# Kernel optimization log

Measured on AMD Instinct MI355X. Metric: run time of the kernel, lower is better.

The kernel has to match this reference:

```python
import jax, jax.numpy as jnp
import numpy as np

D = 1024
N_HEADS = 16
HEAD_DIM = D // N_HEADS
EPS = 1e-09


def setup_inputs() -> dict:
    key = jax.random.key(0)
    ks = jax.random.split(key, 8)
    s = 0.02
    return {
        "x": jax.random.normal(ks[0], (2, 2048, D), jnp.float32),
        "Wq": jax.random.normal(ks[1], (D, D), jnp.float32) * s,
        "Wk": jax.random.normal(ks[2], (D, D), jnp.float32) * s,
        "Wv": jax.random.normal(ks[3], (D, D), jnp.float32) * s,
        "Wo": jax.random.normal(ks[4], (D, D), jnp.float32) * s,
        "W_up": jax.random.normal(ks[5], (4 * D, D), jnp.float32) * s,
        "W_down": jax.random.normal(ks[6], (D, 4 * D), jnp.float32) * s,
        "ln1_mean_scale": jnp.zeros((D,), jnp.float32),
        "ln1_std_scale": jnp.ones((D,), jnp.float32),
        "ln2_mean_scale": jnp.zeros((D,), jnp.float32),
        "ln2_std_scale": jnp.ones((D,), jnp.float32),
    }


def _ln(x, mean_scale, std_scale):
    mean = jnp.mean(x, axis=-1, keepdims=True)
    # torch .var() defaults to unbiased (ddof=1)
    std = jnp.sqrt(jnp.var(x, axis=-1, keepdims=True, ddof=1) + EPS)
    return (x - mean) / std * std_scale + mean_scale


def _attention(x, Wq, Wk, Wv, Wo):
    B, S, _ = x.shape
    # nn.Linear(bias=False): y = x @ W.T
    def heads(W):
        return (x @ W.T).reshape(B, S, N_HEADS, HEAD_DIM).transpose(0, 2, 1, 3)
    Q, K, V = heads(Wq), heads(Wk), heads(Wv)
    scale = jnp.sqrt(jnp.asarray(HEAD_DIM, Q.dtype))
    logits = jnp.einsum('bhqd,bhkd->bhqk', Q, K) / scale  # [B,H,S,S]
    causal = jnp.tril(jnp.ones((S, S), bool))
    logits = jnp.where(causal, logits, -jnp.inf)
    A = jax.nn.softmax(logits, axis=-1)
    preout = jnp.einsum('bhqk,bhkd->bhqd', A, V)  # [B,H,S,hd]
    # Wo.weight.T reshaped to (n_heads, d_head, d_model); per-head out then sum
    W_O = Wo.T.reshape(N_HEADS, HEAD_DIM, D)
    return jnp.einsum('bhsd,hdm->bsm', preout, W_O)


def _mlp(x, W_up, W_down):
    mid = jax.nn.gelu(x @ W_up.T, approximate=False)
    return mid @ W_down.T


def reference(x, Wq, Wk, Wv, Wo, W_up, W_down,
              ln1_mean_scale, ln1_std_scale, ln2_mean_scale, ln2_std_scale):
    x = x + _attention(_ln(x, ln1_mean_scale, ln1_std_scale), Wq, Wk, Wv, Wo)
    x = x + _mlp(_ln(x, ln2_mean_scale, ln2_std_scale), W_up, W_down)
    return x
```

## Files before the change

kernel.cpp:

```cpp
#include <hip/hip_runtime.h>
#include <hip/hip_bf16.h>
#include <cstdint>
#include <cstddef>

#define D_MODEL 1024
#define SEQ     2048
#define NTOK    4096
#define NH      16
#define HD      64

typedef __attribute__((ext_vector_type(8))) short sh8;
typedef __attribute__((ext_vector_type(4))) float f32x4;

#define GLL(g, s) __builtin_amdgcn_global_load_lds(                                   \
    (const __attribute__((address_space(1))) void*)(g),                               \
    (__attribute__((address_space(3))) void*)(s), 16, 0, 0)

__device__ __forceinline__ unsigned short f2b(float f) {
  union { float f; unsigned u; } v; v.f = f;
  unsigned r = v.u + 0x7FFFu + ((v.u >> 16) & 1u);
  return (unsigned short)(r >> 16);
}
__device__ __forceinline__ float b2f(unsigned short h) {
  union { unsigned u; float f; } v; v.u = ((unsigned)h) << 16;
  return v.f;
}

__global__ __launch_bounds__(256) void cast6_kernel(
    const float* __restrict__ q, const float* __restrict__ k, const float* __restrict__ v,
    const float* __restrict__ o, const float* __restrict__ u, const float* __restrict__ d,
    unsigned short* __restrict__ oq, unsigned short* __restrict__ ok,
    unsigned short* __restrict__ ov, unsigned short* __restrict__ oo,
    unsigned short* __restrict__ ou, unsigned short* __restrict__ od) {
  int bid = blockIdx.x;
  const float* src; unsigned short* dst; int base;
  if      (bid < 1024) { src = q; dst = oq; base = bid; }
  else if (bid < 2048) { src = k; dst = ok; base = bid - 1024; }
  else if (bid < 3072) { src = v; dst = ov; base = bid - 2048; }
  else if (bid < 4096) { src = o; dst = oo; base = bid - 3072; }
  else if (bid < 8192) { src = u; dst = ou; base = bid - 4096; }
  else                 { src = d; dst = od; base = bid - 8192; }
  int i = base * 1024 + threadIdx.x * 4;
  float4 vv = *(const float4*)(src + i);
  ushort4 w;
  w.x = f2b(vv.x); w.y = f2b(vv.y); w.z = f2b(vv.z); w.w = f2b(vv.w);
  *(ushort4*)(dst + i) = w;
}

__global__ __launch_bounds__(256) void ln_kernel(const float* __restrict__ x,
                                                 const float* __restrict__ msc,
                                                 const float* __restrict__ ssc,
                                                 unsigned short* __restrict__ out) {
  const int t = blockIdx.x;
  const int tid = threadIdx.x;
  const float4 v = ((const float4*)(x + (size_t)t * D_MODEL))[tid];
  float s = v.x + v.y + v.z + v.w;
  float q = v.x * v.x + v.y * v.y + v.z * v.z + v.w * v.w;
  #pragma unroll
  for (int off = 32; off; off >>= 1) {
    s += __shfl_xor(s, off);
    q += __shfl_xor(q, off);
  }
  __shared__ float sh[8];
  const int w = tid >> 6;
  if ((tid & 63) == 0) { sh[w * 2] = s; sh[w * 2 + 1] = q; }
  __syncthreads();
  s = sh[0] + sh[2] + sh[4] + sh[6];
  q = sh[1] + sh[3] + sh[5] + sh[7];
  const float mean = s * (1.0f / D_MODEL);
  const float var = (q - (float)D_MODEL * mean * mean) * (1.0f / (D_MODEL - 1));
  const float rstd = rsqrtf(var + 1e-9f);
  const float4 ms = ((const float4*)msc)[tid];
  const float4 ss = ((const float4*)ssc)[tid];
  ushort4 o;
  o.x = f2b((v.x - mean) * rstd * ss.x + ms.x);
  o.y = f2b((v.y - mean) * rstd * ss.y + ms.y);
  o.z = f2b((v.z - mean) * rstd * ss.z + ms.z);
  o.w = f2b((v.w - mean) * rstd * ss.w + ms.w);
  ((ushort4*)(out + (size_t)t * D_MODEL))[tid] = o;
}

__global__ __launch_bounds__(256) void reduce_ln_kernel(
    const unsigned short* __restrict__ p0, const unsigned short* __restrict__ p1,
    const float* __restrict__ x, const float* __restrict__ msc,
    const float* __restrict__ ssc, float* __restrict__ out,
    unsigned short* __restrict__ oln) {
  const int t = blockIdx.x;
  const int tid = threadIdx.x;
  const size_t base = (size_t)t * D_MODEL + tid * 4;
  ushort4 a = *(const ushort4*)(p0 + base);
  ushort4 b = *(const ushort4*)(p1 + base);
  float4 xv = *(const float4*)(x + base);
  float4 r;
  r.x = xv.x + b2f(a.x) + b2f(b.x);
  r.y = xv.y + b2f(a.y) + b2f(b.y);
  r.z = xv.z + b2f(a.z) + b2f(b.z);
  r.w = xv.w + b2f(a.w) + b2f(b.w);
  *(float4*)(out + base) = r;
  float s = r.x + r.y + r.z + r.w;
  float q = r.x * r.x + r.y * r.y + r.z * r.z + r.w * r.w;
  #pragma unroll
  for (int off = 32; off; off >>= 1) {
    s += __shfl_xor(s, off);
    q += __shfl_xor(q, off);
  }
  __shared__ float sh[8];
  const int w = tid >> 6;
  if ((tid & 63) == 0) { sh[w * 2] = s; sh[w * 2 + 1] = q; }
  __syncthreads();
  s = sh[0] + sh[2] + sh[4] + sh[6];
  q = sh[1] + sh[3] + sh[5] + sh[7];
  const float mean = s * (1.0f / D_MODEL);
  const float var = (q - (float)D_MODEL * mean * mean) * (1.0f / (D_MODEL - 1));
  const float rstd = rsqrtf(var + 1e-9f);
  const float4 ms = ((const float4*)msc)[tid];
  const float4 ss = ((const float4*)ssc)[tid];
  ushort4 o;
  o.x = f2b((r.x - mean) * rstd * ss.x + ms.x);
  o.y = f2b((r.y - mean) * rstd * ss.y + ms.y);
  o.z = f2b((r.z - mean) * rstd * ss.z + ms.z);
  o.w = f2b((r.w - mean) * rstd * ss.w + ms.w);
  *(ushort4*)(oln + base) = o;
}

__global__ __launch_bounds__(256) void reduce2_kernel(const unsigned short* __restrict__ p0,
                                                      const unsigned short* __restrict__ p1,
                                                      float* __restrict__ out) {
  int i = (blockIdx.x * 256 + threadIdx.x) * 4;
  ushort4 a = *(const ushort4*)(p0 + i);
  ushort4 b = *(const ushort4*)(p1 + i);
  float4 base = *(const float4*)(out + i);
  float4 r;
  r.x = base.x + b2f(a.x) + b2f(b.x);
  r.y = base.y + b2f(a.y) + b2f(b.y);
  r.z = base.z + b2f(a.z) + b2f(b.z);
  r.w = base.w + b2f(a.w) + b2f(b.w);
  *(float4*)(out + i) = r;
}

__global__ __launch_bounds__(256) void attn_combine_kernel(
    unsigned short* __restrict__ p0, const unsigned short* __restrict__ p1,
    const float* __restrict__ l0, const float* __restrict__ l1) {
  int i = (blockIdx.x * 256 + threadIdx.x) * 4;
  const int tok = i >> 10, ch = i & 1023;
  const int b = tok >> 11, s = tok & 2047, h = ch >> 6;
  const int lidx = ((b << 4) + h) * 2048 + s;
  const float inv = 1.0f / (l0[lidx] + l1[lidx]);
  ushort4 a = *(const ushort4*)(p0 + i);
  ushort4 c = *(const ushort4*)(p1 + i);
  ushort4 r;
  r.x = f2b((b2f(a.x) + b2f(c.x)) * inv);
  r.y = f2b((b2f(a.y) + b2f(c.y)) * inv);
  r.z = f2b((b2f(a.z) + b2f(c.z)) * inv);
  r.w = f2b((b2f(a.w) + b2f(c.w)) * inv);
  *(ushort4*)(p0 + i) = r;
}

__global__ __launch_bounds__(256) void vtrans_kernel(const unsigned short* __restrict__ qkv,
                                                     unsigned short* __restrict__ vt) {
  __shared__ unsigned short T[64][72];
  const int st = blockIdx.x;
  const int b  = blockIdx.y >> 4;
  const int dt = blockIdx.y & 15;
  const int tid = threadIdx.x;
  const int s0 = st * 64, d0 = dt * 64;
  const int r = tid >> 2, c0 = (tid & 3) * 16;
  const unsigned short* src = qkv + ((size_t)b * SEQ + s0 + r) * 3072 + 2 * D_MODEL + d0 + c0;
  *(uint4*)&T[r][c0]     = *(const uint4*)(src);
  *(uint4*)&T[r][c0 + 8] = *(const uint4*)(src + 8);
  __syncthreads();
  unsigned short buf[16] __attribute__((aligned(16)));
  #pragma unroll
  for (int j = 0; j < 16; j++) buf[j] = T[c0 + j][r];
  unsigned short* dst = vt + ((size_t)b * D_MODEL + d0 + r) * SEQ + s0 + c0;
  *(uint4*)(dst)     = *(uint4*)&buf[0];
  *(uint4*)(dst + 8) = *(uint4*)&buf[8];
}

template <int EP>
__global__ __launch_bounds__(256) void gemm_nt(const unsigned short* __restrict__ A,
                                               const unsigned short* __restrict__ B,
                                               int N, int LD, int Kext,
                                               unsigned short* __restrict__ Cbf,
                                               unsigned short* __restrict__ Cbf2) {
  __shared__ __align__(16) unsigned short As[128 * 64];
  __shared__ __align__(16) unsigned short Bs[128 * 64];
  const int tid = threadIdx.x;
  const int w = tid >> 6, l = tid & 63, ln = tid & 15, quad = (tid & 63) >> 4;
  const int wr = (w >> 1) * 64, wc = (w & 1) * 64;
  const int m0 = blockIdx.y * 128, n0 = blockIdx.x * 128;
  const int koff = blockIdx.z * Kext;

  const int sr = l >> 3, sc = l & 7;
  const unsigned short* AgS = A + (size_t)(m0 + w * 32 + sr) * LD + koff + ((sc ^ sr) * 8);
  const unsigned short* BgS = B + (size_t)(n0 + w * 32 + sr) * LD + koff + ((sc ^ sr) * 8);
  unsigned short* AsW = &As[(w * 32) * 64];
  unsigned short* BsW = &Bs[(w * 32) * 64];

  f32x4 acc[4][4] = {};

  for (int k0 = 0; k0 < Kext; k0 += 64) {
    __syncthreads();
    #pragma unroll
    for (int off = 0; off < 32; off += 8) {
      GLL(AgS + k0 + (size_t)off * LD, AsW + off * 64);
      GLL(BgS + k0 + (size_t)off * LD, BsW + off * 64);
    }
    __syncthreads();
    sh8 af[2][4], bfr[2][4];
    #pragma unroll
    for (int kk = 0; kk < 2; kk++) {
      #pragma unroll
      for (int i = 0; i < 4; i++)
        af[kk][i]  = *(const sh8*)&As[(wr + i * 16 + ln) * 64 + (((kk * 4 + quad) ^ (ln & 7)) * 8)];
      #pragma unroll
      for (int j = 0; j < 4; j++)
        bfr[kk][j] = *(const sh8*)&Bs[(wc + j * 16 + ln) * 64 + (((kk * 4 + quad) ^ (ln & 7)) * 8)];
    }
    #pragma unroll
    for (int kk = 0; kk < 2; kk++)
      #pragma unroll
      for (int i = 0; i < 4; i++)
        #pragma unroll
        for (int j = 0; j < 4; j++)
          acc[i][j] = __builtin_amdgcn_mfma_f32_16x16x32_bf16(af[kk][i], bfr[kk][j], acc[i][j], 0, 0, 0);
  }

  unsigned short* C = blockIdx.z ? Cbf2 : Cbf;
  #pragma unroll
  for (int i = 0; i < 4; i++) {
    #pragma unroll
    for (int rr = 0; rr < 4; rr++) {
      const int gm = m0 + wr + i * 16 + quad * 4 + rr;
      #pragma unroll
      for (int j = 0; j < 4; j++) {
        const int gn = n0 + wc + j * 16 + ln;
        const float v = acc[i][j][rr];
        const size_t idx = (size_t)gm * N + gn;
        if (EP == 0) {
          C[idx] = f2b(v);
        } else {
          const float g = 0.5f * v * (1.0f + erff(v * 0.70710678118654752f));
          C[idx] = f2b(g);
        }
      }
    }
  }
}

__global__ __launch_bounds__(256) void attn_kernel(const unsigned short* __restrict__ qkv,
                                                   const unsigned short* __restrict__ vt,
                                                   unsigned short* __restrict__ p0,
                                                   unsigned short* __restrict__ p1,
                                                   float* __restrict__ l0,
                                                   float* __restrict__ l1) {
  const int bh = blockIdx.x;
  const int qt = (SEQ / 64 - 1) - blockIdx.y;
  const int z  = blockIdx.z;
  const int b = bh >> 4, h = bh & 15;
  const int tid = threadIdx.x;
  const int w = tid >> 6, l = tid & 63, ln = tid & 15, quad = (tid & 63) >> 4;
  const int q0 = qt * 64;

  __shared__ __align__(16) unsigned short Ks[64 * 64];
  __shared__ __align__(16) unsigned short Vs[64 * 64];
  __shared__ __align__(16) unsigned short Ps[4][16 * 72];

  const size_t rstride = 3 * D_MODEL;
  const unsigned short* Qg = qkv + (size_t)b * SEQ * rstride + h * HD;
  const unsigned short* Kg = Qg + D_MODEL;
  const unsigned short* Vg = vt + ((size_t)b * D_MODEL + h * HD) * SEQ;

  sh8 qf[2];
  {
    const unsigned short* qrow = Qg + (size_t)(q0 + w * 16 + ln) * rstride + quad * 8;
    qf[0] = *(const sh8*)(qrow);
    qf[1] = *(const sh8*)(qrow + 32);
  }

  const int lr3 = l >> 3, lp3 = l & 7;
  const int cS = (lp3 ^ lr3) * 8;
  const unsigned short* KgS = Kg + (size_t)(w * 16 + lr3) * rstride + cS;
  unsigned short* KsW = &Ks[(w * 16) * 64];
  const unsigned short* VgS = Vg + (size_t)(w * 16 + lr3) * SEQ + cS;
  unsigned short* VsW = &Vs[(w * 16) * 64];
  unsigned short* Psw = &Ps[w][0];

  f32x4 o[4] = {};
  float lpart[4] = {0.f, 0.f, 0.f, 0.f};
  const int rbase = q0 + w * 16 + quad * 4;

  auto tile = [&](int kt, bool diag) {
    __syncthreads();
    GLL(KgS + (size_t)(kt * 64) * rstride,     KsW);
    GLL(KgS + (size_t)(kt * 64 + 8) * rstride, KsW + 8 * 64);
    GLL(VgS + kt * 64,           VsW);
    GLL(VgS + 8 * SEQ + kt * 64, VsW + 8 * 64);
    __syncthreads();

    #pragma unroll
    for (int ct = 0; ct < 4; ct++) {
      const int k = ct * 16 + ln;
      f32x4 zz = {};
      zz = __builtin_amdgcn_mfma_f32_16x16x32_bf16(
          qf[0], *(const sh8*)&Ks[k * 64 + ((quad ^ (k & 7)) * 8)], zz, 0, 0, 0);
      zz = __builtin_amdgcn_mfma_f32_16x16x32_bf16(
          qf[1], *(const sh8*)&Ks[k * 64 + (((4 + quad) ^ (k & 7)) * 8)], zz, 0, 0, 0);
      const int cg = kt * 64 + ct * 16 + ln;
      #pragma unroll
      for (int rr = 0; rr < 4; rr++) {
        float e = exp2f(fmaf(zz[rr], 0.18033688011112042f, -5.770780163555853f));
        if (diag && cg > rbase + rr) e = 0.0f;
        lpart[rr] += e;
        Psw[(quad * 4 + rr) * 72 + ct * 16 + ln] = f2b(e);
      }
    }

    #pragma unroll
    for (int kk = 0; kk < 2; kk++) {
      sh8 pf = *(const sh8*)&Psw[ln * 72 + kk * 32 + quad * 8];
      #pragma unroll
      for (int c2 = 0; c2 < 4; c2++) {
        const int d = c2 * 16 + ln;
        sh8 vf = *(const sh8*)&Vs[d * 64 + ((((kk * 4 + quad) ^ (d & 7))) * 8)];
        o[c2] = __builtin_amdgcn_mfma_f32_16x16x32_bf16(pf, vf, o[c2], 0, 0, 0);
      }
    }
  };

  for (int kt = z; kt < qt; kt += 2) tile(kt, false);
  if ((qt & 1) == z) tile(qt, true);

  #pragma unroll
  for (int rr = 0; rr < 4; rr++) {
    #pragma unroll
    for (int off = 1; off < 16; off <<= 1) lpart[rr] += __shfl_xor(lpart[rr], off);
  }

  unsigned short* P = z ? p1 : p0;
  float* L = z ? l1 : l0;
  if (ln == 0) {
    #pragma unroll
    for (int rr = 0; rr < 4; rr++)
      L[((size_t)bh << 11) + q0 + w * 16 + quad * 4 + rr] = lpart[rr];
  }
  #pragma unroll
  for (int rr = 0; rr < 4; rr++) {
    const int row = q0 + w * 16 + quad * 4 + rr;
    const size_t base = ((size_t)b * SEQ + row) * D_MODEL + h * HD;
    #pragma unroll
    for (int c2 = 0; c2 < 4; c2++)
      P[base + c2 * 16 + ln] = f2b(o[c2][rr]);
  }
}

extern "C" void kernel_launch(void* const* d_in, const int* in_sizes, int n_in,
                              void* d_out, int out_size, void* d_ws, size_t ws_size,
                              hipStream_t stream) {
  const float* x    = (const float*)d_in[0];
  const float* Wq   = (const float*)d_in[1];
  const float* Wk   = (const float*)d_in[2];
  const float* Wv   = (const float*)d_in[3];
  const float* Wo   = (const float*)d_in[4];
  const float* Wup  = (const float*)d_in[5];
  const float* Wdn  = (const float*)d_in[6];
  const float* ln1m = (const float*)d_in[7];
  const float* ln1s = (const float*)d_in[8];
  const float* ln2m = (const float*)d_in[9];
  const float* ln2s = (const float*)d_in[10];
  float* out = (float*)d_out;

  unsigned short* ws = (unsigned short*)d_ws;
  size_t off = 0;
  unsigned short* wqkv = ws + off; off += (size_t)3072 * 1024;
  unsigned short* wo   = ws + off; off += (size_t)1024 * 1024;
  unsigned short* wup  = ws + off; off += (size_t)4096 * 1024;
  unsigned short* wdn  = ws + off; off += (size_t)1024 * 4096;
  unsigned short* xln  = ws + off; off += (size_t)NTOK * 1024;
  unsigned short* qkvb = ws + off; off += (size_t)NTOK * 3072;
  unsigned short* pre  = ws + off; off += (size_t)NTOK * 1024;
  unsigned short* mid  = qkvb;
  unsigned short* vtg  = xln;
  unsigned short* po0  = qkvb;
  unsigned short* po1  = qkvb + (size_t)NTOK * 1024;
  unsigned short* pd0  = ws;
  unsigned short* pd1  = xln;
  unsigned short* ap1  = (unsigned short*)out;
  float* al0 = (float*)wqkv;
  float* al1 = al0 + (size_t)2 * NH * SEQ;

  cast6_kernel<<<12288, 256, 0, stream>>>(Wq, Wk, Wv, Wo, Wup, Wdn,
      wqkv, wqkv + (size_t)1024 * 1024, wqkv + (size_t)2 * 1024 * 1024, wo, wup, wdn);

  ln_kernel<<<NTOK, 256, 0, stream>>>(x, ln1m, ln1s, xln);
  gemm_nt<0><<<dim3(24, 32, 1), 256, 0, stream>>>(xln, wqkv, 3072, 1024, 1024, qkvb, nullptr);
  vtrans_kernel<<<dim3(32, 32), 256, 0, stream>>>(qkvb, vtg);
  attn_kernel<<<dim3(2 * NH, SEQ / 64, 2), 256, 0, stream>>>(qkvb, vtg, pre, ap1, al0, al1);
  attn_combine_kernel<<<4096, 256, 0, stream>>>(pre, ap1, al0, al1);
  gemm_nt<0><<<dim3(8, 32, 2), 256, 0, stream>>>(pre, wo, 1024, 1024, 512, po0, po1);
  reduce_ln_kernel<<<NTOK, 256, 0, stream>>>(po0, po1, x, ln2m, ln2s, out, xln);
  gemm_nt<2><<<dim3(32, 32, 1), 256, 0, stream>>>(xln, wup, 4096, 1024, 1024, mid, nullptr);
  gemm_nt<0><<<dim3(8, 32, 2), 256, 0, stream>>>(mid, wdn, 1024, 4096, 2048, pd0, pd1);
  reduce2_kernel<<<4096, 256, 0, stream>>>(pd0, pd1, out);
}
```

Baseline: 361.4 us.

## Replace GEMM with 256-row double-buffered 8-wave kernel and tanh-form GELU

Replaces the 128x128 single-buffered GEMM with a 256xBN tile, 512-thread kernel that double-buffers LDS stages, prefetching two k-tiles ahead with explicit vmcnt waits. It interleaves LDS fragment loads with MFMA groups using setprio and barriers. The aim is to hide global-load latency and raise arithmetic intensity. The up-projection epilogue switches from the erf GELU to a tanh-approximation written as a sigmoid via exp2, which is cheaper but deviates slightly from the exact GELU. The larger tiles reduce the block count, which may hurt load balance on the smaller GEMMs.

```diff
diff --git a/kernel.cpp b/kernel.cpp
--- a/kernel.cpp
+++ b/kernel.cpp
@@ -177,76 +177,137 @@
   *(uint4*)(dst + 8) = *(uint4*)&buf[8];
 }
 
-template <int EP>
-__global__ __launch_bounds__(256) void gemm_nt(const unsigned short* __restrict__ A,
+#define LOADA(ROFF)                                                              \
+  _Pragma("unroll")                                                              \
+  for (int i = 0; i < 4; ++i) {                                                  \
+    const int r_ = wm * 128 + (ROFF) + i * 16 + ln;                              \
+    _Pragma("unroll")                                                            \
+    for (int kk = 0; kk < 2; ++kk)                                               \
+      a[i][kk] = *(const sh8*)&LA[boA + r_ * 64 + (((kk * 4 + quad) ^ (ln & 7)) * 8)]; \
+  }
+
+#define LOADB(DST, ROFF)                                                         \
+  _Pragma("unroll")                                                              \
+  for (int j = 0; j < 2; ++j) {                                                  \
+    const int r_ = wn * (BN / 4) + (ROFF) + j * 16 + ln;                         \
+    _Pragma("unroll")                                                            \
+    for (int kk = 0; kk < 2; ++kk)                                               \
+      DST[j][kk] = *(const sh8*)&LB[boB + r_ * 64 + (((kk * 4 + quad) ^ (ln & 7)) * 8)]; \
+  }
+
+#define MFMA16(IB, JB, BB)                                                       \
+  asm volatile("s_waitcnt lgkmcnt(0)" ::: "memory");                             \
+  __builtin_amdgcn_sched_barrier(0);                                             \
+  __builtin_amdgcn_s_setprio(1);                                                 \
+  _Pragma("unroll")                                                              \
+  for (int kk = 0; kk < 2; ++kk)                                                 \
+    _Pragma("unroll")                                                            \
+    for (int i = 0; i < 4; ++i)                                                  \
+      _Pragma("unroll")                                                          \
+      for (int j = 0; j < 2; ++j)                                                \
+        acc[(IB) + i][(JB) + j] = __builtin_amdgcn_mfma_f32_16x16x32_bf16(       \
+            a[i][kk], BB[j][kk], acc[(IB) + i][(JB) + j], 0, 0, 0);              \
+  __builtin_amdgcn_s_setprio(0);                                                 \
+  __builtin_amdgcn_s_barrier();
+
+template <int BN, int EP>
+__global__ __launch_bounds__(512) void gemm256(const unsigned short* __restrict__ A,
                                                const unsigned short* __restrict__ B,
                                                int N, int LD, int Kext,
-                                               unsigned short* __restrict__ Cbf,
-                                               unsigned short* __restrict__ Cbf2) {
-  __shared__ __align__(16) unsigned short As[128 * 64];
-  __shared__ __align__(16) unsigned short Bs[128 * 64];
+                                               unsigned short* __restrict__ C0,
+                                               unsigned short* __restrict__ C1) {
+  constexpr int NJ    = BN / 64;
+  constexpr int BROWS = BN / 8;
+  __shared__ __align__(16) unsigned short LA[2 * 256 * 64];
+  __shared__ __align__(16) unsigned short LB[2 * BN * 64];
   const int tid = threadIdx.x;
-  const int w = tid >> 6, l = tid & 63, ln = tid & 15, quad = (tid & 63) >> 4;
-  const int wr = (w >> 1) * 64, wc = (w & 1) * 64;
-  const int m0 = blockIdx.y * 128, n0 = blockIdx.x * 128;
+  const int wid = tid >> 6, l = tid & 63, ln = l & 15, quad = l >> 4;
+  const int wm = wid >> 2, wn = wid & 3;
+  const int m0 = blockIdx.y * 256, n0 = blockIdx.x * BN;
   const int koff = blockIdx.z * Kext;
+  const int nt = Kext >> 6;
 
   const int sr = l >> 3, sc = l & 7;
-  const unsigned short* AgS = A + (size_t)(m0 + w * 32 + sr) * LD + koff + ((sc ^ sr) * 8);
-  const unsigned short* BgS = B + (size_t)(n0 + w * 32 + sr) * LD + koff + ((sc ^ sr) * 8);
-  unsigned short* AsW = &As[(w * 32) * 64];
-  unsigned short* BsW = &Bs[(w * 32) * 64];
-
-  f32x4 acc[4][4] = {};
-
-  for (int k0 = 0; k0 < Kext; k0 += 64) {
-    __syncthreads();
-    #pragma unroll
-    for (int off = 0; off < 32; off += 8) {
-      GLL(AgS + k0 + (size_t)off * LD, AsW + off * 64);
-      GLL(BgS + k0 + (size_t)off * LD, BsW + off * 64);
-    }
-    __syncthreads();
-    sh8 af[2][4], bfr[2][4];
-    #pragma unroll
-    for (int kk = 0; kk < 2; kk++) {
+  const unsigned short* AgS = A + (size_t)(m0 + wid * 32 + sr) * LD + koff + (sc ^ sr) * 8;
+  const unsigned short* BgS = B + (size_t)(n0 + wid * BROWS + sr) * LD + koff + (sc ^ sr) * 8;
+
+  auto stage = [&](int tt, int bsel) {
+    const unsigned short* as = AgS + tt * 64;
+    const unsigned short* bs = BgS + tt * 64;
+    unsigned short* ad = &LA[bsel * (256 * 64) + (wid * 32) * 64];
+    unsigned short* bd = &LB[bsel * (BN * 64) + (wid * BROWS) * 64];
+    #pragma unroll
+    for (int off = 0; off < 32; off += 8)
+      GLL(as + (size_t)off * LD, ad + off * 64);
+    #pragma unroll
+    for (int off = 0; off < BROWS; off += 8)
+      GLL(bs + (size_t)off * LD, bd + off * 64);
+  };
+
+  f32x4 acc[8][NJ] = {};
+
+  stage(0, 0);
+  stage(1, 1);
+  if constexpr (BN == 256) asm volatile("s_waitcnt vmcnt(8)" ::: "memory");
+  else                     asm volatile("s_waitcnt vmcnt(6)" ::: "memory");
+  __builtin_amdgcn_s_barrier();
+  __builtin_amdgcn_sched_barrier(0);
+
+  for (int t = 0; t < nt; ++t) {
+    const int boA = (t & 1) * (256 * 64);
+    const int boB = (t & 1) * (BN * 64);
+    sh8 a[4][2], bA[2][2];
+    LOADA(0)
+    LOADB(bA, 0)
+    MFMA16(0, 0, bA)
+    if constexpr (BN == 256) {
+      sh8 bB[2][2];
+      LOADB(bB, 32)
+      MFMA16(0, 2, bB)
+      LOADA(64)
+      MFMA16(4, 2, bB)
+      LOADB(bA, 0)
+      MFMA16(4, 0, bA)
+    } else {
+      LOADA(64)
+      MFMA16(4, 0, bA)
+    }
+    if (t + 2 < nt) {
+      stage(t + 2, t & 1);
+      if constexpr (BN == 256) asm volatile("s_waitcnt vmcnt(8)" ::: "memory");
+      else                     asm volatile("s_waitcnt vmcnt(6)" ::: "memory");
+    } else if (t + 1 < nt) {
+      asm volatile("s_waitcnt vmcnt(0)" ::: "memory");
+    }
+    if (t + 1 < nt) {
+      __builtin_amdgcn_s_barrier();
+      __builtin_amdgcn_sched_barrier(0);
+    }
+  }
+
+  unsigned short* C = blockIdx.z ? C1 : C0;
+  #pragma unroll
+  for (int i = 0; i < 8; ++i) {
+    #pragma unroll
+    for (int rr = 0; rr < 4; ++rr) {
+      const int gm = m0 + wm * 128 + i * 16 + quad * 4 + rr;
       #pragma unroll
-      for (int i = 0; i < 4; i++)
-        af[kk][i]  = *(const sh8*)&As[(wr + i * 16 + ln) * 64 + (((kk * 4 + quad) ^ (ln & 7)) * 8)];
-      #pragma unroll
-      for (int j = 0; j < 4; j++)
-        bfr[kk][j] = *(const sh8*)&Bs[(wc + j * 16 + ln) * 64 + (((kk * 4 + quad) ^ (ln & 7)) * 8)];
-    }
-    #pragma unroll
-    for (int kk = 0; kk < 2; kk++)
-      #pragma unroll
-      for (int i = 0; i < 4; i++)
-        #pragma unroll
-        for (int j = 0; j < 4; j++)
-          acc[i][j] = __builtin_amdgcn_mfma_f32_16x16x32_bf16(af[kk][i], bfr[kk][j], acc[i][j], 0, 0, 0);
-  }
-
-  unsigned short* C = blockIdx.z ? Cbf2 : Cbf;
-  #pragma unroll
-  for (int i = 0; i < 4; i++) {
-    #pragma unroll
-    for (int rr = 0; rr < 4; rr++) {
-      const int gm = m0 + wr + i * 16 + quad * 4 + rr;
-      #pragma unroll
-      for (int j = 0; j < 4; j++) {
-        const int gn = n0 + wc + j * 16 + ln;
-        const float v = acc[i][j][rr];
-        const size_t idx = (size_t)gm * N + gn;
-        if (EP == 0) {
-          C[idx] = f2b(v);
-        } else {
-          const float g = 0.5f * v * (1.0f + erff(v * 0.70710678118654752f));
-          C[idx] = f2b(g);
+      for (int j = 0; j < NJ; ++j) {
+        const int gn = n0 + wn * (BN / 4) + j * 16 + ln;
+        float v = acc[i][j][rr];
+        if (EP == 1) {
+          const float vc = fminf(v, 8.0f);
+          const float e = exp2f(2.3021906f * fmaf(0.044715f * vc * vc, vc, vc));
+          v = v * e / (e + 1.0f);
         }
+        C[(size_t)gm * N + gn] = f2b(v);
       }
     }
   }
 }
+#undef LOADA
+#undef LOADB
+#undef MFMA16
 
 __global__ __launch_bounds__(256) void attn_kernel(const unsigned short* __restrict__ qkv,
                                                    const unsigned short* __restrict__ vt,
@@ -393,13 +454,13 @@
       wqkv, wqkv + (size_t)1024 * 1024, wqkv + (size_t)2 * 1024 * 1024, wo, wup, wdn);
 
   ln_kernel<<<NTOK, 256, 0, stream>>>(x, ln1m, ln1s, xln);
-  gemm_nt<0><<<dim3(24, 32, 1), 256, 0, stream>>>(xln, wqkv, 3072, 1024, 1024, qkvb, nullptr);
+  gemm256<256, 0><<<dim3(12, 16, 1), 512, 0, stream>>>(xln, wqkv, 3072, 1024, 1024, qkvb, nullptr);
   vtrans_kernel<<<dim3(32, 32), 256, 0, stream>>>(qkvb, vtg);
   attn_kernel<<<dim3(2 * NH, SEQ / 64, 2), 256, 0, stream>>>(qkvb, vtg, pre, ap1, al0, al1);
   attn_combine_kernel<<<4096, 256, 0, stream>>>(pre, ap1, al0, al1);
-  gemm_nt<0><<<dim3(8, 32, 2), 256, 0, stream>>>(pre, wo, 1024, 1024, 512, po0, po1);
+  gemm256<128, 0><<<dim3(8, 16, 2), 512, 0, stream>>>(pre, wo, 1024, 1024, 512, po0, po1);
   reduce_ln_kernel<<<NTOK, 256, 0, stream>>>(po0, po1, x, ln2m, ln2s, out, xln);
-  gemm_nt<2><<<dim3(32, 32, 1), 256, 0, stream>>>(xln, wup, 4096, 1024, 1024, mid, nullptr);
-  gemm_nt<0><<<dim3(8, 32, 2), 256, 0, stream>>>(mid, wdn, 1024, 4096, 2048, pd0, pd1);
+  gemm256<256, 1><<<dim3(16, 16, 1), 512, 0, stream>>>(xln, wup, 4096, 1024, 1024, mid, nullptr);
+  gemm256<128, 0><<<dim3(8, 16, 2), 512, 0, stream>>>(mid, wdn, 1024, 4096, 2048, pd0, pd1);
   reduce2_kernel<<<4096, 256, 0, stream>>>(pd0, pd1, out);
 }
```

Result: no change. 359.0 us (-0.6%).
